# Optimization experiments

Hardware: AMD Instinct MI355X
Metric: run time of the kernel (lower is better)

Reference implementation:

```python
import jax, jax.numpy as jnp
import numpy as np

N_NODES = 50000
N_EDGES = 800000
D_IN = 128
D_OUT = 128


def setup_inputs() -> dict:
    key = jax.random.key(0)
    k1, k2, k3, k4, k5 = jax.random.split(key, 5)
    H = jax.random.normal(k1, (N_NODES, D_IN), dtype=jnp.float32)
    stdv = 1.0 / np.sqrt(D_OUT)
    W = jax.random.uniform(k2, (D_IN, D_OUT), dtype=jnp.float32, minval=-stdv, maxval=stdv)
    bias = jnp.zeros((D_OUT,), dtype=jnp.float32)
    edge_vals = jax.random.uniform(k3, (N_EDGES,), dtype=jnp.float32)
    edge_rows = jax.random.randint(k4, (N_EDGES,), 0, N_NODES, dtype=jnp.int32)
    edge_cols = jax.random.randint(k5, (N_EDGES,), 0, N_NODES, dtype=jnp.int32)
    return {"H": H, "W": W, "bias": bias, "edge_vals": edge_vals,
            "edge_rows": edge_rows, "edge_cols": edge_cols}


def reference(H, W, bias, edge_vals, edge_rows, edge_cols):
    # H' = relu(A @ (H W) + b), A given as COO edge list (rows, cols, vals)
    n = H.shape[0]
    HW = H @ W  # [N, D_out]
    # SpMM: out[r] = sum_{e: row(e)=r} val(e) * HW[col(e)]
    msgs = edge_vals[:, None] * HW[edge_cols]  # [E, D_out]
    out = jax.ops.segment_sum(msgs, edge_rows, num_segments=n)
    out = out + bias
    return jax.nn.relu(out)
```

## Files before the change

kernel.cpp:

```cpp
#include <hip/hip_runtime.h>

#define D 128
#define BM 64
#define NBS 256
#define BINSH 6
#define MAXBINS 1024
#define CAPB 1536
#define EBUF 3200

typedef __attribute__((ext_vector_type(8))) short bf16x8;
typedef __attribute__((ext_vector_type(4))) float f32x4;

__device__ __forceinline__ unsigned short f2bf(float f) {
    unsigned u = __float_as_uint(f);
    u = (u + 0x7FFFu + ((u >> 16) & 1u)) >> 16;
    return (unsigned short)u;
}
__device__ __forceinline__ float bf2f(unsigned short h) {
    return __uint_as_float(((unsigned)h) << 16);
}

__global__ __launch_bounds__(128) void k_prepw(const float* __restrict__ W,
                                               unsigned short* __restrict__ Wt) {
    int nn = blockIdx.x, k = threadIdx.x;
    Wt[nn * D + k] = f2bf(W[k * D + nn]);
}

__global__ __launch_bounds__(256) void k_gemm_bsort(const float* __restrict__ H,
                                                    const unsigned short* __restrict__ Wt,
                                                    unsigned short* __restrict__ HWb,
                                                    int n,
                                                    const int* __restrict__ rows,
                                                    const int* __restrict__ cols,
                                                    const float* __restrict__ vals,
                                                    int2* __restrict__ segs,
                                                    int* __restrict__ offtT,
                                                    int E, int nbins, int chunk,
                                                    int gblocks) {
    __shared__ union {
        struct { unsigned short sA[BM * 64]; unsigned short sB[D * 64]; } g;
        struct { int hist[MAXBINS]; int excl[MAXBINS + 1]; int wsum[4];
                 int2 ebuf[EBUF]; } s;
    } u;
    const int tid = threadIdx.x;

    if (blockIdx.x < (unsigned)gblocks) {
        unsigned short* sA = u.g.sA;
        unsigned short* sB = u.g.sB;
        const int row0 = blockIdx.x * BM;
        const int w = tid >> 6, l = tid & 63;
        const int lr = l & 15, lq = l >> 4;

        f32x4 acc[8];
#pragma unroll
        for (int ct = 0; ct < 8; ++ct) acc[ct] = (f32x4){0.f, 0.f, 0.f, 0.f};

#pragma unroll
        for (int kt = 0; kt < 2; ++kt) {
            if (kt) __syncthreads();
#pragma unroll
            for (int s = 0; s < 4; ++s) {
                int idx = s * 256 + tid;
                int r = idx >> 3, cc = idx & 7;
                bf16x8 v = *reinterpret_cast<const bf16x8*>(&Wt[(size_t)r * D + kt * 64 + cc * 8]);
                *reinterpret_cast<bf16x8*>(&sB[r * 64 + ((cc ^ (r & 7)) * 8)]) = v;
            }
#pragma unroll
            for (int s = 0; s < 2; ++s) {
                int idx = s * 256 + tid;
                int r = idx >> 3, cc = idx & 7;
                int row = row0 + r;
                float4 u0 = make_float4(0.f, 0.f, 0.f, 0.f), u1 = u0;
                if (row < n) {
                    const float4* p = reinterpret_cast<const float4*>(
                        &H[(size_t)row * D + kt * 64 + cc * 8]);
                    u0 = p[0]; u1 = p[1];
                }
                bf16x8 v;
                v[0] = (short)f2bf(u0.x); v[1] = (short)f2bf(u0.y);
                v[2] = (short)f2bf(u0.z); v[3] = (short)f2bf(u0.w);
                v[4] = (short)f2bf(u1.x); v[5] = (short)f2bf(u1.y);
                v[6] = (short)f2bf(u1.z); v[7] = (short)f2bf(u1.w);
                *reinterpret_cast<bf16x8*>(&sA[r * 64 + ((cc ^ (r & 7)) * 8)]) = v;
            }
            __syncthreads();

#pragma unroll
            for (int ks = 0; ks < 2; ++ks) {
                const int arow = w * 16 + lr;
                const int acc_c = (ks * 4 + lq) ^ (arow & 7);
                bf16x8 a = *reinterpret_cast<const bf16x8*>(&sA[arow * 64 + acc_c * 8]);
#pragma unroll
                for (int ct = 0; ct < 8; ++ct) {
                    const int brow = ct * 16 + lr;
                    const int bcc = (ks * 4 + lq) ^ (brow & 7);
                    bf16x8 b = *reinterpret_cast<const bf16x8*>(&sB[brow * 64 + bcc * 8]);
                    acc[ct] = __builtin_amdgcn_mfma_f32_16x16x32_bf16(b, a, acc[ct], 0, 0, 0);
                }
            }
        }

        int row = row0 + w * 16 + lr;
        if (row < n) {
#pragma unroll
            for (int ct = 0; ct < 8; ++ct) {
                ushort4 o;
                o.x = f2bf(acc[ct][0]); o.y = f2bf(acc[ct][1]);
                o.z = f2bf(acc[ct][2]); o.w = f2bf(acc[ct][3]);
                *reinterpret_cast<ushort4*>(&HWb[(size_t)row * D + ct * 16 + lq * 4]) = o;
            }
        }
        return;
    }

    int* hist = u.s.hist;
    int* excl = u.s.excl;
    int* wsum = u.s.wsum;
    int2* ebuf = u.s.ebuf;
    const int p = blockIdx.x - gblocks;
    const int s = p * chunk;
    int epos = s + chunk; if (epos > E) epos = E;
    const int len = (epos > s) ? (epos - s) : 0;

    for (int i = tid; i < nbins; i += 256) hist[i] = 0;
    __syncthreads();
    if (len > 0) {
        const int t0 = s + (len & ~3);
        for (int base = s + tid * 4; base + 4 <= epos; base += 1024) {
            int4 r4 = *reinterpret_cast<const int4*>(&rows[base]);
            atomicAdd(&hist[r4.x >> BINSH], 1);
            atomicAdd(&hist[r4.y >> BINSH], 1);
            atomicAdd(&hist[r4.z >> BINSH], 1);
            atomicAdd(&hist[r4.w >> BINSH], 1);
        }
        for (int e = t0 + tid; e < epos; e += 256)
            atomicAdd(&hist[rows[e] >> BINSH], 1);
    }
    __syncthreads();

    int b0 = tid * 4;
    int h0 = 0, h1 = 0, h2 = 0, h3 = 0, sum = 0;
    if (b0 < nbins) {
        h0 = hist[b0];
        h1 = (b0 + 1 < nbins) ? hist[b0 + 1] : 0;
        h2 = (b0 + 2 < nbins) ? hist[b0 + 2] : 0;
        h3 = (b0 + 3 < nbins) ? hist[b0 + 3] : 0;
        sum = h0 + h1 + h2 + h3;
    }
    {
        int lane = tid & 63, w = tid >> 6;
        int inc = sum;
#pragma unroll
        for (int o = 1; o < 64; o <<= 1) {
            int t = __shfl_up(inc, o);
            if (lane >= o) inc += t;
        }
        if (lane == 63) wsum[w] = inc;
        __syncthreads();
        int wex = 0;
        for (int j = 0; j < w; ++j) wex += wsum[j];
        int cur = wex + inc - sum;
        if (b0 < nbins) {
            excl[b0] = cur; hist[b0] = cur; cur += h0;
            if (b0 + 1 < nbins) { excl[b0 + 1] = cur; hist[b0 + 1] = cur; cur += h1; }
            if (b0 + 2 < nbins) { excl[b0 + 2] = cur; hist[b0 + 2] = cur; cur += h2; }
            if (b0 + 3 < nbins) { excl[b0 + 3] = cur; hist[b0 + 3] = cur; cur += h3; }
        }
        if (tid == 255) excl[nbins] = len;
    }
    __syncthreads();

    if (len > 0) {
        const int t0 = s + (len & ~3);
        for (int base = s + tid * 4; base + 4 <= epos; base += 1024) {
            int4 r4 = *reinterpret_cast<const int4*>(&rows[base]);
            int4 c4 = *reinterpret_cast<const int4*>(&cols[base]);
            float4 v4 = *reinterpret_cast<const float4*>(&vals[base]);
            int q0 = atomicAdd(&hist[r4.x >> BINSH], 1);
            int q1 = atomicAdd(&hist[r4.y >> BINSH], 1);
            int q2 = atomicAdd(&hist[r4.z >> BINSH], 1);
            int q3 = atomicAdd(&hist[r4.w >> BINSH], 1);
            ebuf[q0] = make_int2(((r4.x & 63) << 16) | c4.x, __float_as_int(v4.x));
            ebuf[q1] = make_int2(((r4.y & 63) << 16) | c4.y, __float_as_int(v4.y));
            ebuf[q2] = make_int2(((r4.z & 63) << 16) | c4.z, __float_as_int(v4.z));
            ebuf[q3] = make_int2(((r4.w & 63) << 16) | c4.w, __float_as_int(v4.w));
        }
        for (int e = t0 + tid; e < epos; e += 256) {
            int r = rows[e];
            int q = atomicAdd(&hist[r >> BINSH], 1);
            ebuf[q] = make_int2(((r & 63) << 16) | cols[e], __float_as_int(vals[e]));
        }
    }
    __syncthreads();

    for (int i = tid; i < len; i += 256)
        segs[(size_t)p * chunk + i] = ebuf[i];
    for (int i = tid; i <= nbins; i += 256)
        offtT[(size_t)i * NBS + p] = p * chunk + excl[i];
}

__global__ __launch_bounds__(512) void k_spmm(const unsigned short* __restrict__ HWb,
                                              const int* __restrict__ offtT,
                                              const int2* __restrict__ segs,
                                              const float* __restrict__ bias,
                                              float* __restrict__ out, int n, int nbins) {
    __shared__ int2 ent[CAPB];
    __shared__ int2 sent[CAPB];
    __shared__ int lcnt[64];
    __shared__ int loff[64];
    __shared__ int lcur[64];
    __shared__ int wsum[8];
    __shared__ int total_s;
    const int b = blockIdx.x;
    const int tid = threadIdx.x;

    int o0 = 0, c = 0;
    if (tid < NBS) {
        o0 = offtT[(size_t)b * NBS + tid];
        int o1 = offtT[(size_t)(b + 1) * NBS + tid];
        c = o1 - o0;
    }
    {
        int lane = tid & 63, w = tid >> 6;
        int inc = c;
#pragma unroll
        for (int o = 1; o < 64; o <<= 1) {
            int t = __shfl_up(inc, o);
            if (lane >= o) inc += t;
        }
        if (lane == 63) wsum[w] = inc;
        __syncthreads();
        int wex = 0;
        for (int j = 0; j < w; ++j) wex += wsum[j];
        int myoff = wex + inc - c;
        if (tid == 511) total_s = wex + inc;
        for (int j = 0; j < c; ++j) {
            int q = myoff + j;
            if (q < CAPB) ent[q] = segs[o0 + j];
        }
    }
    if (tid < 64) lcnt[tid] = 0;
    __syncthreads();
    int cnt = total_s;
    if (cnt > CAPB) cnt = CAPB;

    for (int i = tid; i < cnt; i += 512)
        atomicAdd(&lcnt[((unsigned)ent[i].x) >> 16], 1);
    __syncthreads();
    if (tid < 64) {
        int v = lcnt[tid];
        int inc = v;
#pragma unroll
        for (int o = 1; o < 64; o <<= 1) {
            int t = __shfl_up(inc, o);
            if (tid >= o) inc += t;
        }
        loff[tid] = inc - v;
        lcur[tid] = inc - v;
    }
    __syncthreads();
    for (int i = tid; i < cnt; i += 512) {
        int2 e = ent[i];
        int q = atomicAdd(&lcur[((unsigned)e.x) >> 16], 1);
        sent[q] = e;
    }
    __syncthreads();

    const int w = tid >> 6, lane = tid & 63;
    const unsigned c2 = 2 * lane;
    const float2 bb = *reinterpret_cast<const float2*>(&bias[c2]);

    for (int rr = w; rr < 64; rr += 8) {
        int row = b * 64 + rr;
        if (row >= n) break;
        int s = loff[rr];
        int deg = lcnt[rr];
        float a0 = 0.f, a1 = 0.f, b0 = 0.f, b1 = 0.f;
        int t = 0;
        for (; t + 8 <= deg; t += 8) {
            int2 e0 = sent[s + t],     e1 = sent[s + t + 1];
            int2 e2 = sent[s + t + 2], e3 = sent[s + t + 3];
            int2 e4 = sent[s + t + 4], e5 = sent[s + t + 5];
            int2 e6 = sent[s + t + 6], e7 = sent[s + t + 7];
            unsigned m0 = *reinterpret_cast<const unsigned*>(&HWb[(size_t)(e0.x & 0xFFFF) * D + c2]);
            unsigned m1 = *reinterpret_cast<const unsigned*>(&HWb[(size_t)(e1.x & 0xFFFF) * D + c2]);
            unsigned m2 = *reinterpret_cast<const unsigned*>(&HWb[(size_t)(e2.x & 0xFFFF) * D + c2]);
            unsigned m3 = *reinterpret_cast<const unsigned*>(&HWb[(size_t)(e3.x & 0xFFFF) * D + c2]);
            unsigned m4 = *reinterpret_cast<const unsigned*>(&HWb[(size_t)(e4.x & 0xFFFF) * D + c2]);
            unsigned m5 = *reinterpret_cast<const unsigned*>(&HWb[(size_t)(e5.x & 0xFFFF) * D + c2]);
            unsigned m6 = *reinterpret_cast<const unsigned*>(&HWb[(size_t)(e6.x & 0xFFFF) * D + c2]);
            unsigned m7 = *reinterpret_cast<const unsigned*>(&HWb[(size_t)(e7.x & 0xFFFF) * D + c2]);
            float v0 = __int_as_float(e0.y), v1 = __int_as_float(e1.y);
            float v2 = __int_as_float(e2.y), v3 = __int_as_float(e3.y);
            float v4 = __int_as_float(e4.y), v5 = __int_as_float(e5.y);
            float v6 = __int_as_float(e6.y), v7 = __int_as_float(e7.y);
            a0 += v0 * bf2f((unsigned short)(m0 & 0xFFFF));
            a1 += v0 * bf2f((unsigned short)(m0 >> 16));
            b0 += v1 * bf2f((unsigned short)(m1 & 0xFFFF));
            b1 += v1 * bf2f((unsigned short)(m1 >> 16));
            a0 += v2 * bf2f((unsigned short)(m2 & 0xFFFF));
            a1 += v2 * bf2f((unsigned short)(m2 >> 16));
            b0 += v3 * bf2f((unsigned short)(m3 & 0xFFFF));
            b1 += v3 * bf2f((unsigned short)(m3 >> 16));
            a0 += v4 * bf2f((unsigned short)(m4 & 0xFFFF));
            a1 += v4 * bf2f((unsigned short)(m4 >> 16));
            b0 += v5 * bf2f((unsigned short)(m5 & 0xFFFF));
            b1 += v5 * bf2f((unsigned short)(m5 >> 16));
            a0 += v6 * bf2f((unsigned short)(m6 & 0xFFFF));
            a1 += v6 * bf2f((unsigned short)(m6 >> 16));
            b0 += v7 * bf2f((unsigned short)(m7 & 0xFFFF));
            b1 += v7 * bf2f((unsigned short)(m7 >> 16));
        }
        for (; t < deg; ++t) {
            int2 e = sent[s + t];
            unsigned m = *reinterpret_cast<const unsigned*>(&HWb[(size_t)(e.x & 0xFFFF) * D + c2]);
            float v = __int_as_float(e.y);
            a0 += v * bf2f((unsigned short)(m & 0xFFFF));
            a1 += v * bf2f((unsigned short)(m >> 16));
        }
        float2 o;
        o.x = fmaxf(a0 + b0 + bb.x, 0.f);
        o.y = fmaxf(a1 + b1 + bb.y, 0.f);
        *reinterpret_cast<float2*>(&out[(size_t)row * D + c2]) = o;
    }
}

__global__ void k_init_bias(const float* __restrict__ bias, float* __restrict__ out, int n) {
    int i = blockIdx.x * blockDim.x + threadIdx.x;
    if (i < n * D) out[i] = bias[i & (D - 1)];
}
__global__ void k_scatter(const unsigned short* __restrict__ HWb, const int* __restrict__ rows,
                          const int* __restrict__ cols, const float* __restrict__ vals,
                          float* __restrict__ out, int E) {
    int e = blockIdx.x * 2 + (threadIdx.x >> 7);
    int j = threadIdx.x & (D - 1);
    if (e < E) {
        int r = rows[e];
        int c = cols[e];
        float v = vals[e];
        atomicAdd(&out[(size_t)r * D + j], v * bf2f(HWb[(size_t)c * D + j]));
    }
}
__global__ void k_relu(float* __restrict__ out, int n) {
    int i = blockIdx.x * blockDim.x + threadIdx.x;
    if (i < n * D) out[i] = fmaxf(out[i], 0.f);
}

extern "C" void kernel_launch(void* const* d_in, const int* in_sizes, int n_in,
                              void* d_out, int out_size, void* d_ws, size_t ws_size,
                              hipStream_t stream) {
    const float* H         = (const float*)d_in[0];
    const float* W         = (const float*)d_in[1];
    const float* bias      = (const float*)d_in[2];
    const float* edge_vals = (const float*)d_in[3];
    const int*   edge_rows = (const int*)d_in[4];
    const int*   edge_cols = (const int*)d_in[5];
    float* out = (float*)d_out;

    const int n = in_sizes[0] / D;
    const int E = in_sizes[3];
    const int gblocks = (n + BM - 1) / BM;
    const int nbins = (n + 63) >> BINSH;
    int chunk = (E + NBS - 1) / NBS;
    chunk = (chunk + 3) & ~3;

    char* ws = (char*)d_ws;
    unsigned short* HWb = (unsigned short*)ws; ws += (size_t)n * D * sizeof(unsigned short);
    unsigned short* Wt  = (unsigned short*)ws; ws += (size_t)D * D * sizeof(unsigned short);
    int2* segs = (int2*)ws;          ws += (size_t)NBS * chunk * sizeof(int2);
    int* offtT = (int*)ws;           ws += (size_t)(nbins + 1) * NBS * sizeof(int);
    size_t need_full = (size_t)(ws - (char*)d_ws);

    k_prepw<<<D, D, 0, stream>>>(W, Wt);

    if (ws_size >= need_full && n < 65536 && nbins <= MAXBINS && chunk <= EBUF) {
        k_gemm_bsort<<<gblocks + NBS, 256, 0, stream>>>(H, Wt, HWb, n,
                                                        edge_rows, edge_cols, edge_vals,
                                                        segs, offtT, E, nbins, chunk, gblocks);
        k_spmm<<<nbins, 512, 0, stream>>>(HWb, offtT, segs, bias, out, n, nbins);
    } else {
        k_gemm_bsort<<<gblocks, 256, 0, stream>>>(H, Wt, HWb, n,
                                                  edge_rows, edge_cols, edge_vals,
                                                  (int2*)d_ws, (int*)d_ws, 0, nbins, chunk, gblocks);
        k_init_bias<<<((size_t)n * D + 255) / 256, 256, 0, stream>>>(bias, out, n);
        k_scatter<<<(E + 1) / 2, 256, 0, stream>>>(HWb, edge_rows, edge_cols, edge_vals, out, E);
        k_relu<<<((size_t)n * D + 255) / 256, 256, 0, stream>>>(out, n);
    }
}
```

Before: 65.06 us.

## Scatter bin-sorted edges directly to global and interleave two rows in SpMM

The bin-sort blocks no longer stage edges in a shared-memory buffer before copying them out. They write each edge straight to its global segment position, which removes the LDS buffer, a barrier and the copy loop. The union is also smaller, which may raise occupancy of the fused GEMM/sort kernel, but the global stores become scattered. The SpMM kernel now has each wave process two rows at once, with interleaved gathers feeding separate accumulators, to keep more independent memory loads in flight.

After: 64.07 us. Within noise of the previous version (-1.5%).

```diff
diff --git a/kernel.cpp b/kernel.cpp
--- a/kernel.cpp
+++ b/kernel.cpp
@@ -6,7 +6,6 @@
 #define BINSH 6
 #define MAXBINS 1024
 #define CAPB 1536
-#define EBUF 3200
 
 typedef __attribute__((ext_vector_type(8))) short bf16x8;
 typedef __attribute__((ext_vector_type(4))) float f32x4;
@@ -39,8 +38,7 @@
                                                     int gblocks) {
     __shared__ union {
         struct { unsigned short sA[BM * 64]; unsigned short sB[D * 64]; } g;
-        struct { int hist[MAXBINS]; int excl[MAXBINS + 1]; int wsum[4];
-                 int2 ebuf[EBUF]; } s;
+        struct { int hist[MAXBINS]; int excl[MAXBINS + 1]; int wsum[4]; } s;
     } u;
     const int tid = threadIdx.x;
 
@@ -116,7 +114,6 @@
     int* hist = u.s.hist;
     int* excl = u.s.excl;
     int* wsum = u.s.wsum;
-    int2* ebuf = u.s.ebuf;
     const int p = blockIdx.x - gblocks;
     const int s = p * chunk;
     int epos = s + chunk; if (epos > E) epos = E;
@@ -171,6 +168,7 @@
     __syncthreads();
 
     if (len > 0) {
+        int2* segp = segs + (size_t)p * chunk;
         const int t0 = s + (len & ~3);
         for (int base = s + tid * 4; base + 4 <= epos; base += 1024) {
             int4 r4 = *reinterpret_cast<const int4*>(&rows[base]);
@@ -180,24 +178,29 @@
             int q1 = atomicAdd(&hist[r4.y >> BINSH], 1);
             int q2 = atomicAdd(&hist[r4.z >> BINSH], 1);
             int q3 = atomicAdd(&hist[r4.w >> BINSH], 1);
-            ebuf[q0] = make_int2(((r4.x & 63) << 16) | c4.x, __float_as_int(v4.x));
-            ebuf[q1] = make_int2(((r4.y & 63) << 16) | c4.y, __float_as_int(v4.y));
-            ebuf[q2] = make_int2(((r4.z & 63) << 16) | c4.z, __float_as_int(v4.z));
-            ebuf[q3] = make_int2(((r4.w & 63) << 16) | c4.w, __float_as_int(v4.w));
+            segp[q0] = make_int2(((r4.x & 63) << 16) | c4.x, __float_as_int(v4.x));
+            segp[q1] = make_int2(((r4.y & 63) << 16) | c4.y, __float_as_int(v4.y));
+            segp[q2] = make_int2(((r4.z & 63) << 16) | c4.z, __float_as_int(v4.z));
+            segp[q3] = make_int2(((r4.w & 63) << 16) | c4.w, __float_as_int(v4.w));
         }
         for (int e = t0 + tid; e < epos; e += 256) {
             int r = rows[e];
             int q = atomicAdd(&hist[r >> BINSH], 1);
-            ebuf[q] = make_int2(((r & 63) << 16) | cols[e], __float_as_int(vals[e]));
-        }
-    }
-    __syncthreads();
-
-    for (int i = tid; i < len; i += 256)
-        segs[(size_t)p * chunk + i] = ebuf[i];
+            segp[q] = make_int2(((r & 63) << 16) | cols[e], __float_as_int(vals[e]));
+        }
+    }
     for (int i = tid; i <= nbins; i += 256)
         offtT[(size_t)i * NBS + p] = p * chunk + excl[i];
 }
+
+#define GATH(e, p0, p1)                                                              \
+    {                                                                                \
+        unsigned mm = *reinterpret_cast<const unsigned*>(                            \
+            &HWb[(size_t)((e).x & 0xFFFF) * D + c2]);                                \
+        float vv = __int_as_float((e).y);                                            \
+        p0 += vv * bf2f((unsigned short)(mm & 0xFFFF));                              \
+        p1 += vv * bf2f((unsigned short)(mm >> 16));                                 \
+    }
 
 __global__ __launch_bounds__(512) void k_spmm(const unsigned short* __restrict__ HWb,
                                               const int* __restrict__ offtT,
@@ -270,58 +273,53 @@
     const unsigned c2 = 2 * lane;
     const float2 bb = *reinterpret_cast<const float2*>(&bias[c2]);
 
-    for (int rr = w; rr < 64; rr += 8) {
-        int row = b * 64 + rr;
-        if (row >= n) break;
-        int s = loff[rr];
-        int deg = lcnt[rr];
-        float a0 = 0.f, a1 = 0.f, b0 = 0.f, b1 = 0.f;
+    for (int rr = w; rr < 64; rr += 16) {
+        const int rA = rr, rB = rr + 8;
+        const int rowA = b * 64 + rA, rowB = b * 64 + rB;
+        int sa = loff[rA], da = (rowA < n) ? lcnt[rA] : 0;
+        int sb = loff[rB], db = (rowB < n) ? lcnt[rB] : 0;
+        float a0 = 0.f, a1 = 0.f, p0 = 0.f, p1 = 0.f;
+        float g0 = 0.f, g1 = 0.f, q0 = 0.f, q1 = 0.f;
+        int m = da < db ? da : db;
         int t = 0;
-        for (; t + 8 <= deg; t += 8) {
-            int2 e0 = sent[s + t],     e1 = sent[s + t + 1];
-            int2 e2 = sent[s + t + 2], e3 = sent[s + t + 3];
-            int2 e4 = sent[s + t + 4], e5 = sent[s + t + 5];
-            int2 e6 = sent[s + t + 6], e7 = sent[s + t + 7];
-            unsigned m0 = *reinterpret_cast<const unsigned*>(&HWb[(size_t)(e0.x & 0xFFFF) * D + c2]);
-            unsigned m1 = *reinterpret_cast<const unsigned*>(&HWb[(size_t)(e1.x & 0xFFFF) * D + c2]);
-            unsigned m2 = *reinterpret_cast<const unsigned*>(&HWb[(size_t)(e2.x & 0xFFFF) * D + c2]);
-            unsigned m3 = *reinterpret_cast<const unsigned*>(&HWb[(size_t)(e3.x & 0xFFFF) * D + c2]);
-            unsigned m4 = *reinterpret_cast<const unsigned*>(&HWb[(size_t)(e4.x & 0xFFFF) * D + c2]);
-            unsigned m5 = *reinterpret_cast<const unsigned*>(&HWb[(size_t)(e5.x & 0xFFFF) * D + c2]);
-            unsigned m6 = *reinterpret_cast<const unsigned*>(&HWb[(size_t)(e6.x & 0xFFFF) * D + c2]);
-            unsigned m7 = *reinterpret_cast<const unsigned*>(&HWb[(size_t)(e7.x & 0xFFFF) * D + c2]);
-            float v0 = __int_as_float(e0.y), v1 = __int_as_float(e1.y);
-            float v2 = __int_as_float(e2.y), v3 = __int_as_float(e3.y);
-            float v4 = __int_as_float(e4.y), v5 = __int_as_float(e5.y);
-            float v6 = __int_as_float(e6.y), v7 = __int_as_float(e7.y);
-            a0 += v0 * bf2f((unsigned short)(m0 & 0xFFFF));
-            a1 += v0 * bf2f((unsigned short)(m0 >> 16));
-            b0 += v1 * bf2f((unsigned short)(m1 & 0xFFFF));
-            b1 += v1 * bf2f((unsigned short)(m1 >> 16));
-            a0 += v2 * bf2f((unsigned short)(m2 & 0xFFFF));
-            a1 += v2 * bf2f((unsigned short)(m2 >> 16));
-            b0 += v3 * bf2f((unsigned short)(m3 & 0xFFFF));
-            b1 += v3 * bf2f((unsigned short)(m3 >> 16));
-            a0 += v4 * bf2f((unsigned short)(m4 & 0xFFFF));
-            a1 += v4 * bf2f((unsigned short)(m4 >> 16));
-            b0 += v5 * bf2f((unsigned short)(m5 & 0xFFFF));
-            b1 += v5 * bf2f((unsigned short)(m5 >> 16));
-            a0 += v6 * bf2f((unsigned short)(m6 & 0xFFFF));
-            a1 += v6 * bf2f((unsigned short)(m6 >> 16));
-            b0 += v7 * bf2f((unsigned short)(m7 & 0xFFFF));
-            b1 += v7 * bf2f((unsigned short)(m7 >> 16));
-        }
-        for (; t < deg; ++t) {
-            int2 e = sent[s + t];
-            unsigned m = *reinterpret_cast<const unsigned*>(&HWb[(size_t)(e.x & 0xFFFF) * D + c2]);
-            float v = __int_as_float(e.y);
-            a0 += v * bf2f((unsigned short)(m & 0xFFFF));
-            a1 += v * bf2f((unsigned short)(m >> 16));
-        }
-        float2 o;
-        o.x = fmaxf(a0 + b0 + bb.x, 0.f);
-        o.y = fmaxf(a1 + b1 + bb.y, 0.f);
-        *reinterpret_cast<float2*>(&out[(size_t)row * D + c2]) = o;
+        for (; t + 4 <= m; t += 4) {
+            int2 eA0 = sent[sa + t],     eA1 = sent[sa + t + 1];
+            int2 eA2 = sent[sa + t + 2], eA3 = sent[sa + t + 3];
+            int2 eB0 = sent[sb + t],     eB1 = sent[sb + t + 1];
+            int2 eB2 = sent[sb + t + 2], eB3 = sent[sb + t + 3];
+            GATH(eA0, a0, a1); GATH(eB0, g0, g1);
+            GATH(eA1, p0, p1); GATH(eB1, q0, q1);
+            GATH(eA2, a0, a1); GATH(eB2, g0, g1);
+            GATH(eA3, p0, p1); GATH(eB3, q0, q1);
+        }
+        int ta = t, tb = t;
+        for (; ta + 4 <= da; ta += 4) {
+            int2 e0 = sent[sa + ta],     e1 = sent[sa + ta + 1];
+            int2 e2 = sent[sa + ta + 2], e3 = sent[sa + ta + 3];
+            GATH(e0, a0, a1); GATH(e1, p0, p1);
+            GATH(e2, a0, a1); GATH(e3, p0, p1);
+        }
+        for (; ta < da; ++ta) { int2 e = sent[sa + ta]; GATH(e, a0, a1); }
+        for (; tb + 4 <= db; tb += 4) {
+            int2 e0 = sent[sb + tb],     e1 = sent[sb + tb + 1];
+            int2 e2 = sent[sb + tb + 2], e3 = sent[sb + tb + 3];
+            GATH(e0, g0, g1); GATH(e1, q0, q1);
+            GATH(e2, g0, g1); GATH(e3, q0, q1);
+        }
+        for (; tb < db; ++tb) { int2 e = sent[sb + tb]; GATH(e, g0, g1); }
+
+        if (rowA < n) {
+            float2 o;
+            o.x = fmaxf(a0 + p0 + bb.x, 0.f);
+            o.y = fmaxf(a1 + p1 + bb.y, 0.f);
+            *reinterpret_cast<float2*>(&out[(size_t)rowA * D + c2]) = o;
+        }
+        if (rowB < n) {
+            float2 o;
+            o.x = fmaxf(g0 + q0 + bb.x, 0.f);
+            o.y = fmaxf(g1 + q1 + bb.y, 0.f);
+            *reinterpret_cast<float2*>(&out[(size_t)rowB * D + c2]) = o;
+        }
     }
 }
 
@@ -373,7 +371,7 @@
 
     k_prepw<<<D, D, 0, stream>>>(W, Wt);
 
-    if (ws_size >= need_full && n < 65536 && nbins <= MAXBINS && chunk <= EBUF) {
+    if (ws_size >= need_full && n < 65536 && nbins <= MAXBINS) {
         k_gemm_bsort<<<gblocks + NBS, 256, 0, stream>>>(H, Wt, HWb, n,
                                                         edge_rows, edge_cols, edge_vals,
                                                         segs, offtT, E, nbins, chunk, gblocks);
```
